# Kernel optimization log

Measured on AMD Instinct MI355X. Metric: run time of the kernel, lower is better.

## Reference

```python
import jax, jax.numpy as jnp
import numpy as np

DIM = 1024
SEQ = 32768
BATCH = 1
MIN_ACTIVE = 0.01
MAX_ACTIVE = 0.1
KMAX = int(MAX_ACTIVE * DIM) + 1  # static upper bound on dynamic k (<= 102)
EPS = 1e-6


def setup_inputs() -> dict:
    key = jax.random.key(0)
    ks = jax.random.split(key, 7)
    h = DIM // 8
    s = 0.02
    return {
        "x": jax.random.normal(ks[0], (BATCH, SEQ, DIM), jnp.float32),
        # complexity_net: Linear(dim, dim//8) -> GELU -> Linear(dim//8, 1) -> Sigmoid
        "w1": jax.random.normal(ks[1], (DIM, h), jnp.float32) * s,
        "b1": jnp.zeros((h,), jnp.float32),
        "w2": jax.random.normal(ks[2], (h, 1), jnp.float32) * s,
        "b2": jnp.zeros((1,), jnp.float32),
        # gate_net: Linear(dim, dim)
        "wg": jax.random.normal(ks[3], (DIM, DIM), jnp.float32) * s,
        "bg": jnp.zeros((DIM,), jnp.float32),
        # running stats (eval mode: used for normalization, not updated)
        "running_mean": jax.random.normal(ks[4], (DIM,), jnp.float32) * 0.1,
        "running_var": jax.random.uniform(ks[5], (DIM,), jnp.float32, minval=0.5, maxval=1.5),
    }


def reference(x, w1, b1, w2, b2, wg, bg, running_mean, running_var):
    # complexity from seq-mean pooled features -> scalar in (0,1)
    pooled = x.mean(axis=1, keepdims=True)                      # (B,1,D)
    hid = jax.nn.gelu(pooled @ w1 + b1, approximate=False)      # torch GELU is exact erf
    complexity = jax.nn.sigmoid(hid @ w2 + b2)                  # (B,1,1)
    active_ratio = MIN_ACTIVE + (MAX_ACTIVE - MIN_ACTIVE) * complexity
    # torch .int() truncates; clamp(min=1). B==1 so k is effectively scalar.
    k = jnp.clip((active_ratio * DIM).astype(jnp.int32), 1, KMAX)  # (B,1,1)

    importance = jnp.abs(x @ wg + bg)                           # (B,S,D)
    importance = (importance - running_mean) / (jnp.sqrt(running_var) + EPS)

    # dynamic-k topk via static-KMAX top_k + threshold at the k-th largest value
    topk_vals, _ = jax.lax.top_k(importance, KMAX)              # (B,S,KMAX)
    idx = jnp.broadcast_to((k - 1).astype(jnp.int32), (x.shape[0], x.shape[1], 1))
    kth = jnp.take_along_axis(topk_vals, idx, axis=-1)          # (B,S,1)
    mask = (importance >= kth).astype(x.dtype)                  # (B,S,D), non-differentiable
    mask = jax.lax.stop_gradient(mask)

    # straight-through combine: forward = x*mask, backward passes grad to all of x
    sparse_x = x * mask + (x - jax.lax.stop_gradient(x)) * (1.0 - mask)

    complexity_mean = complexity.mean()
    active_ratio_mean = active_ratio.mean()
    active_neurons = k.astype(jnp.float32).mean()
    return sparse_x, complexity_mean, active_ratio_mean, active_neurons
```

## Files before the change

### kernel.cpp

```cpp
#include <hip/hip_runtime.h>
#include <cstdint>
#include <cstddef>

#define SEQ 32768
#define DIM 1024
#define HID 128
#define KMAXV 103

using f4 = __attribute__((ext_vector_type(4))) float;
using f2 = __attribute__((ext_vector_type(2))) float;

__global__ __launch_bounds__(256) void pool_partial(const float* __restrict__ x,
                                                    double* __restrict__ part) {
    const int b = blockIdx.x;
    const int t = threadIdx.x;
    const int r0 = b * 128;
    double s0 = 0.0, s1 = 0.0, s2 = 0.0, s3 = 0.0;
    for (int r = 0; r < 128; ++r) {
        const float* row = x + (size_t)(r0 + r) * DIM;
        s0 += (double)row[t];
        s1 += (double)row[t + 256];
        s2 += (double)row[t + 512];
        s3 += (double)row[t + 768];
    }
    double* p = part + (size_t)b * DIM;
    p[t] = s0; p[t + 256] = s1; p[t + 512] = s2; p[t + 768] = s3;
}

__global__ __launch_bounds__(1024) void tiny_net(const double* __restrict__ part,
                                                 const float* __restrict__ w1,
                                                 const float* __restrict__ b1,
                                                 const float* __restrict__ w2,
                                                 const float* __restrict__ b2,
                                                 float* __restrict__ out_scalars,
                                                 int* __restrict__ kout) {
    __shared__ double pooled[DIM];
    __shared__ double hidv[HID];
    const int t = threadIdx.x;

    double s = 0.0;
    for (int b = 0; b < 256; ++b) s += part[(size_t)b * DIM + t];
    pooled[t] = s / (double)SEQ;
    __syncthreads();

    if (t < HID) {
        double h = (double)b1[t];
        for (int d = 0; d < DIM; ++d) h += pooled[d] * (double)w1[d * HID + t];
        h = 0.5 * h * (1.0 + erf(h * 0.70710678118654752440));
        hidv[t] = h;
    }
    __syncthreads();

    if (t == 0) {
        double z = (double)b2[0];
        for (int j = 0; j < HID; ++j) z += hidv[j] * (double)w2[j];
        double c = 1.0 / (1.0 + exp(-z));
        double ar = 0.01 + 0.09 * c;
        int k = (int)(ar * (double)DIM);
        if (k < 1) k = 1;
        if (k > KMAXV) k = KMAXV;
        out_scalars[0] = (float)c;
        out_scalars[1] = (float)ar;
        out_scalars[2] = (float)k;
        *kout = k;
    }
}

#define BM 16
#define CBLOCK 512

__device__ __forceinline__ void fma_step(const float* __restrict__ xp,
                                         f2 w0, f2 w1, f2 w2, f2 w3,
                                         f2 acc[16]) {
#pragma unroll
    for (int m = 0; m < 16; ++m) {
        const f2 xab = *(const f2*)(xp + m * DIM);
        const f2 xcd = *(const f2*)(xp + m * DIM + 2);
        asm("v_pk_fma_f32 %0, %1, %2, %0 op_sel:[0,0,0] op_sel_hi:[0,1,1]"
            : "+v"(acc[m]) : "s"(xab), "v"(w0));
        asm("v_pk_fma_f32 %0, %1, %2, %0 op_sel:[1,0,0] op_sel_hi:[1,1,1]"
            : "+v"(acc[m]) : "s"(xab), "v"(w1));
        asm("v_pk_fma_f32 %0, %1, %2, %0 op_sel:[0,0,0] op_sel_hi:[0,1,1]"
            : "+v"(acc[m]) : "s"(xcd), "v"(w2));
        asm("v_pk_fma_f32 %0, %1, %2, %0 op_sel:[1,0,0] op_sel_hi:[1,1,1]"
            : "+v"(acc[m]) : "s"(xcd), "v"(w3));
    }
}

template<int K0, int K1>
__device__ __forceinline__ void panel_acc(const float* __restrict__ x,
                                          const float* __restrict__ wbase,
                                          int row0, f2 acc[16]) {
#pragma unroll
    for (int m = 0; m < 16; ++m) { acc[m][0] = 0.0f; acc[m][1] = 0.0f; }

    const float* xbase = x + (size_t)row0 * DIM;

    f2 a0 = *(const f2*)(wbase + (size_t)(K0 + 0) * DIM);
    f2 a1 = *(const f2*)(wbase + (size_t)(K0 + 1) * DIM);
    f2 a2 = *(const f2*)(wbase + (size_t)(K0 + 2) * DIM);
    f2 a3 = *(const f2*)(wbase + (size_t)(K0 + 3) * DIM);

    for (int kk0 = K0; kk0 < K1; kk0 += 8) {
        const f2 b0 = *(const f2*)(wbase + (size_t)(kk0 + 4) * DIM);
        const f2 b1 = *(const f2*)(wbase + (size_t)(kk0 + 5) * DIM);
        const f2 b2v = *(const f2*)(wbase + (size_t)(kk0 + 6) * DIM);
        const f2 b3 = *(const f2*)(wbase + (size_t)(kk0 + 7) * DIM);

        fma_step(xbase + kk0, a0, a1, a2, a3, acc);

        const int kn = (kk0 + 8 < K1) ? kk0 + 8 : K0;
        const f2 c0 = *(const f2*)(wbase + (size_t)(kn + 0) * DIM);
        const f2 c1 = *(const f2*)(wbase + (size_t)(kn + 1) * DIM);
        const f2 c2v = *(const f2*)(wbase + (size_t)(kn + 2) * DIM);
        const f2 c3 = *(const f2*)(wbase + (size_t)(kn + 3) * DIM);

        fma_step(xbase + kk0 + 4, b0, b1, b2v, b3, acc);

        a0 = c0; a1 = c1; a2 = c2v; a3 = c3;
    }
}

__global__ __launch_bounds__(CBLOCK) void panel1_kernel(const float* __restrict__ x,
                                                        const float* __restrict__ wg,
                                                        float* __restrict__ out) {
    const int t = threadIdx.x;
    const int c2 = t << 1;
    const int row0 = blockIdx.x * BM;

    f2 pacc[16];
    panel_acc<0, 384>(x, wg + c2, row0, pacc);

#pragma unroll
    for (int m = 0; m < 16; ++m)
        *(f2*)(out + (size_t)(row0 + m) * DIM + c2) = pacc[m];
}

__global__ __launch_bounds__(CBLOCK) void panel2_kernel(const float* __restrict__ x,
                                                        const float* __restrict__ wg,
                                                        float* __restrict__ out) {
    const int t = threadIdx.x;
    const int c2 = t << 1;
    const int row0 = blockIdx.x * BM;

    f2 pacc[16];
    panel_acc<384, 704>(x, wg + c2, row0, pacc);

#pragma unroll
    for (int m = 0; m < 16; ++m) {
        float* op = out + (size_t)(row0 + m) * DIM + c2;
        f2 d = *(const f2*)op;
        d[0] = d[0] + pacc[m][0];
        d[1] = d[1] + pacc[m][1];
        *(f2*)op = d;
    }
}

__global__ __launch_bounds__(CBLOCK) void panel3_kernel(const float* __restrict__ x,
                                                        const float* __restrict__ wg,
                                                        const float* __restrict__ bg,
                                                        const float* __restrict__ rm,
                                                        const float* __restrict__ rv,
                                                        const int* __restrict__ kptr,
                                                        float* __restrict__ out) {
    __shared__ float lbuf[8 * DIM];

    const int t = threadIdx.x;
    const int c2 = t << 1;
    const int row0 = blockIdx.x * BM;

    f2 pacc[16];
    panel_acc<704, 1024>(x, wg + c2, row0, pacc);

    float dot[16][2];
#pragma unroll
    for (int m = 0; m < 16; ++m) {
        const f2 d = *(const f2*)(out + (size_t)(row0 + m) * DIM + c2);
        dot[m][0] = d[0] + pacc[m][0];
        dot[m][1] = d[1] + pacc[m][1];
    }

    const f2 vbg = *(const f2*)(bg + c2);
    const f2 vrm = *(const f2*)(rm + c2);
    const f2 vrv = *(const f2*)(rv + c2);
    f2 vden;
    vden[0] = sqrtf(vrv[0]) + 1e-6f;
    vden[1] = sqrtf(vrv[1]) + 1e-6f;

    f2 imp[16];
#pragma unroll
    for (int m = 0; m < 16; ++m) {
        imp[m][0] = (fabsf(dot[m][0] + vbg[0]) - vrm[0]) / vden[0];
        imp[m][1] = (fabsf(dot[m][1] + vbg[1]) - vrm[1]) / vden[1];
    }

    int kval = *kptr;
    if (kval < 1) kval = 1;
    if (kval > DIM) kval = DIM;

    float (*selbuf)[DIM] = (float (*)[DIM])lbuf;

    for (int ch = 0; ch < 2; ++ch) {
        __syncthreads();
#pragma unroll
        for (int m = 0; m < 8; ++m)
            *(f2*)(&selbuf[m][c2]) = imp[ch * 8 + m];
        __syncthreads();

        const int w = t >> 6;
        const int l = t & 63;
        const size_t srow = (size_t)(row0 + ch * 8 + w);

        unsigned keys[16];
#pragma unroll
        for (int j = 0; j < 4; ++j) {
            const f4 v = *(const f4*)(&selbuf[w][4 * l + 256 * j]);
#pragma unroll
            for (int i = 0; i < 4; ++i) {
                const unsigned u = __float_as_uint(v[i]);
                keys[j * 4 + i] = (u & 0x80000000u) ? ~u : (u | 0x80000000u);
            }
        }

        unsigned pref = 0u;
        for (int b = 31; b >= 0; --b) {
            const unsigned tt = pref | (1u << b);
            int cnt = 0;
#pragma unroll
            for (int j = 0; j < 16; ++j) cnt += (keys[j] >= tt) ? 1 : 0;
#pragma unroll
            for (int off = 32; off >= 1; off >>= 1) cnt += __shfl_xor(cnt, off, 64);
            if (cnt >= kval) pref = tt;
        }

        const float* xr = x + srow * DIM;
        float* orow = out + srow * DIM;
#pragma unroll
        for (int j = 0; j < 4; ++j) {
            const f4 xv = *(const f4*)(xr + 4 * l + 256 * j);
            f4 o;
#pragma unroll
            for (int i = 0; i < 4; ++i) o[i] = (keys[j * 4 + i] >= pref) ? xv[i] : 0.0f;
            *(f4*)(orow + 4 * l + 256 * j) = o;
        }
    }
}

extern "C" void kernel_launch(void* const* d_in, const int* in_sizes, int n_in,
                              void* d_out, int out_size, void* d_ws, size_t ws_size,
                              hipStream_t stream) {
    const float* x  = (const float*)d_in[0];
    const float* w1 = (const float*)d_in[1];
    const float* b1 = (const float*)d_in[2];
    const float* w2 = (const float*)d_in[3];
    const float* b2 = (const float*)d_in[4];
    const float* wg = (const float*)d_in[5];
    const float* bg = (const float*)d_in[6];
    const float* rm = (const float*)d_in[7];
    const float* rv = (const float*)d_in[8];
    float* out = (float*)d_out;

    double* part = (double*)d_ws;
    int* kptr = (int*)((char*)d_ws + (size_t)256 * DIM * sizeof(double));

    pool_partial<<<256, 256, 0, stream>>>(x, part);
    tiny_net<<<1, 1024, 0, stream>>>(part, w1, b1, w2, b2,
                                     out + (size_t)SEQ * DIM, kptr);
    panel1_kernel<<<SEQ / BM, CBLOCK, 0, stream>>>(x, wg, out);
    panel2_kernel<<<SEQ / BM, CBLOCK, 0, stream>>>(x, wg, out);
    panel3_kernel<<<SEQ / BM, CBLOCK, 0, stream>>>(x, wg, bg, rm, rv, kptr, out);
}
```

Before: 0.9999 ms.

## Fuse three K-panel GEMM kernels into one kernel with 1024-thread blocks

Replaces three panel kernels with one fused kernel. The kernels previously wrote and reread partial dot products through the output buffer between launches; the fused kernel keeps the accumulation in registers and runs the normalization and top-k selection in the same kernel. Block size doubles to 1024 threads, with two 8-row groups per block, so each thread holds 8 accumulators instead of 16 and loads x as float4. Costs include lower occupancy per CU and the x loads possibly becoming scalar loads from a uniform row group, so the register and scheduling behavior may change.

```diff
diff --git a/kernel.cpp b/kernel.cpp
--- a/kernel.cpp
+++ b/kernel.cpp
@@ -67,15 +67,16 @@
 }
 
 #define BM 16
-#define CBLOCK 512
-
-__device__ __forceinline__ void fma_step(const float* __restrict__ xp,
-                                         f2 w0, f2 w1, f2 w2, f2 w3,
-                                         f2 acc[16]) {
-#pragma unroll
-    for (int m = 0; m < 16; ++m) {
-        const f2 xab = *(const f2*)(xp + m * DIM);
-        const f2 xcd = *(const f2*)(xp + m * DIM + 2);
+#define CBLOCK 1024
+
+__device__ __forceinline__ void fma_step2(const float* __restrict__ xp,
+                                          f2 w0, f2 w1, f2 w2, f2 w3,
+                                          f2 acc[8]) {
+#pragma unroll
+    for (int m = 0; m < 8; ++m) {
+        const f4 xq = *(const f4*)(xp + m * DIM);
+        const f2 xab = __builtin_shufflevector(xq, xq, 0, 1);
+        const f2 xcd = __builtin_shufflevector(xq, xq, 2, 3);
         asm("v_pk_fma_f32 %0, %1, %2, %0 op_sel:[0,0,0] op_sel_hi:[0,1,1]"
             : "+v"(acc[m]) : "s"(xab), "v"(w0));
         asm("v_pk_fma_f32 %0, %1, %2, %0 op_sel:[1,0,0] op_sel_hi:[1,1,1]"
@@ -88,13 +89,11 @@
 }
 
 template<int K0, int K1>
-__device__ __forceinline__ void panel_acc(const float* __restrict__ x,
-                                          const float* __restrict__ wbase,
-                                          int row0, f2 acc[16]) {
-#pragma unroll
-    for (int m = 0; m < 16; ++m) { acc[m][0] = 0.0f; acc[m][1] = 0.0f; }
-
-    const float* xbase = x + (size_t)row0 * DIM;
+__device__ __forceinline__ void panel_acc2(const float* __restrict__ xbase,
+                                           const float* __restrict__ wbase,
+                                           f2 acc[8]) {
+#pragma unroll
+    for (int m = 0; m < 8; ++m) { acc[m][0] = 0.0f; acc[m][1] = 0.0f; }
 
     f2 a0 = *(const f2*)(wbase + (size_t)(K0 + 0) * DIM);
     f2 a1 = *(const f2*)(wbase + (size_t)(K0 + 1) * DIM);
@@ -107,7 +106,7 @@
         const f2 b2v = *(const f2*)(wbase + (size_t)(kk0 + 6) * DIM);
         const f2 b3 = *(const f2*)(wbase + (size_t)(kk0 + 7) * DIM);
 
-        fma_step(xbase + kk0, a0, a1, a2, a3, acc);
+        fma_step2(xbase + kk0, a0, a1, a2, a3, acc);
 
         const int kn = (kk0 + 8 < K1) ? kk0 + 8 : K0;
         const f2 c0 = *(const f2*)(wbase + (size_t)(kn + 0) * DIM);
@@ -115,69 +114,48 @@
         const f2 c2v = *(const f2*)(wbase + (size_t)(kn + 2) * DIM);
         const f2 c3 = *(const f2*)(wbase + (size_t)(kn + 3) * DIM);
 
-        fma_step(xbase + kk0 + 4, b0, b1, b2v, b3, acc);
+        fma_step2(xbase + kk0 + 4, b0, b1, b2v, b3, acc);
 
         a0 = c0; a1 = c1; a2 = c2v; a3 = c3;
     }
 }
 
-__global__ __launch_bounds__(CBLOCK) void panel1_kernel(const float* __restrict__ x,
-                                                        const float* __restrict__ wg,
-                                                        float* __restrict__ out) {
+__global__ __launch_bounds__(CBLOCK) void fused_kernel(const float* __restrict__ x,
+                                                       const float* __restrict__ wg,
+                                                       const float* __restrict__ bg,
+                                                       const float* __restrict__ rm,
+                                                       const float* __restrict__ rv,
+                                                       const int* __restrict__ kptr,
+                                                       float* __restrict__ out) {
+    __shared__ float selbuf[BM][DIM];
+
     const int t = threadIdx.x;
-    const int c2 = t << 1;
-    const int row0 = blockIdx.x * BM;
-
-    f2 pacc[16];
-    panel_acc<0, 384>(x, wg + c2, row0, pacc);
-
-#pragma unroll
-    for (int m = 0; m < 16; ++m)
-        *(f2*)(out + (size_t)(row0 + m) * DIM + c2) = pacc[m];
-}
-
-__global__ __launch_bounds__(CBLOCK) void panel2_kernel(const float* __restrict__ x,
-                                                        const float* __restrict__ wg,
-                                                        float* __restrict__ out) {
-    const int t = threadIdx.x;
-    const int c2 = t << 1;
-    const int row0 = blockIdx.x * BM;
-
-    f2 pacc[16];
-    panel_acc<384, 704>(x, wg + c2, row0, pacc);
-
-#pragma unroll
-    for (int m = 0; m < 16; ++m) {
-        float* op = out + (size_t)(row0 + m) * DIM + c2;
-        f2 d = *(const f2*)op;
-        d[0] = d[0] + pacc[m][0];
-        d[1] = d[1] + pacc[m][1];
-        *(f2*)op = d;
-    }
-}
-
-__global__ __launch_bounds__(CBLOCK) void panel3_kernel(const float* __restrict__ x,
-                                                        const float* __restrict__ wg,
-                                                        const float* __restrict__ bg,
-                                                        const float* __restrict__ rm,
-                                                        const float* __restrict__ rv,
-                                                        const int* __restrict__ kptr,
-                                                        float* __restrict__ out) {
-    __shared__ float lbuf[8 * DIM];
-
-    const int t = threadIdx.x;
-    const int c2 = t << 1;
-    const int row0 = blockIdx.x * BM;
-
-    f2 pacc[16];
-    panel_acc<704, 1024>(x, wg + c2, row0, pacc);
-
-    float dot[16][2];
-#pragma unroll
-    for (int m = 0; m < 16; ++m) {
-        const f2 d = *(const f2*)(out + (size_t)(row0 + m) * DIM + c2);
-        dot[m][0] = d[0] + pacc[m][0];
-        dot[m][1] = d[1] + pacc[m][1];
+    const int c2 = (t & 511) << 1;
+    const int rg = __builtin_amdgcn_readfirstlane(t >> 9);
+    const int row0 = blockIdx.x * BM + rg * 8;
+
+    const float* xbase = x + (size_t)row0 * DIM;
+    const float* wbase = wg + c2;
+
+    f2 pacc[8];
+    f2 dot[8];
+
+    panel_acc2<0, 384>(xbase, wbase, pacc);
+#pragma unroll
+    for (int m = 0; m < 8; ++m) dot[m] = pacc[m];
+
+    panel_acc2<384, 704>(xbase, wbase, pacc);
+#pragma unroll
+    for (int m = 0; m < 8; ++m) {
+        dot[m][0] = dot[m][0] + pacc[m][0];
+        dot[m][1] = dot[m][1] + pacc[m][1];
+    }
+
+    panel_acc2<704, 1024>(xbase, wbase, pacc);
+#pragma unroll
+    for (int m = 0; m < 8; ++m) {
+        dot[m][0] = dot[m][0] + pacc[m][0];
+        dot[m][1] = dot[m][1] + pacc[m][1];
     }
 
     const f2 vbg = *(const f2*)(bg + c2);
@@ -187,62 +165,55 @@
     vden[0] = sqrtf(vrv[0]) + 1e-6f;
     vden[1] = sqrtf(vrv[1]) + 1e-6f;
 
-    f2 imp[16];
-#pragma unroll
-    for (int m = 0; m < 16; ++m) {
-        imp[m][0] = (fabsf(dot[m][0] + vbg[0]) - vrm[0]) / vden[0];
-        imp[m][1] = (fabsf(dot[m][1] + vbg[1]) - vrm[1]) / vden[1];
+#pragma unroll
+    for (int m = 0; m < 8; ++m) {
+        f2 v;
+        v[0] = (fabsf(dot[m][0] + vbg[0]) - vrm[0]) / vden[0];
+        v[1] = (fabsf(dot[m][1] + vbg[1]) - vrm[1]) / vden[1];
+        *(f2*)(&selbuf[rg * 8 + m][c2]) = v;
     }
 
     int kval = *kptr;
     if (kval < 1) kval = 1;
     if (kval > DIM) kval = DIM;
 
-    float (*selbuf)[DIM] = (float (*)[DIM])lbuf;
-
-    for (int ch = 0; ch < 2; ++ch) {
-        __syncthreads();
-#pragma unroll
-        for (int m = 0; m < 8; ++m)
-            *(f2*)(&selbuf[m][c2]) = imp[ch * 8 + m];
-        __syncthreads();
-
-        const int w = t >> 6;
-        const int l = t & 63;
-        const size_t srow = (size_t)(row0 + ch * 8 + w);
-
-        unsigned keys[16];
-#pragma unroll
-        for (int j = 0; j < 4; ++j) {
-            const f4 v = *(const f4*)(&selbuf[w][4 * l + 256 * j]);
-#pragma unroll
-            for (int i = 0; i < 4; ++i) {
-                const unsigned u = __float_as_uint(v[i]);
-                keys[j * 4 + i] = (u & 0x80000000u) ? ~u : (u | 0x80000000u);
-            }
+    __syncthreads();
+
+    const int w = t >> 6;
+    const int l = t & 63;
+    const size_t srow = (size_t)(blockIdx.x * BM + w);
+
+    unsigned keys[16];
+#pragma unroll
+    for (int j = 0; j < 4; ++j) {
+        const f4 v = *(const f4*)(&selbuf[w][4 * l + 256 * j]);
+#pragma unroll
+        for (int i = 0; i < 4; ++i) {
+            const unsigned u = __float_as_uint(v[i]);
+            keys[j * 4 + i] = (u & 0x80000000u) ? ~u : (u | 0x80000000u);
         }
-
-        unsigned pref = 0u;
-        for (int b = 31; b >= 0; --b) {
-            const unsigned tt = pref | (1u << b);
-            int cnt = 0;
-#pragma unroll
-            for (int j = 0; j < 16; ++j) cnt += (keys[j] >= tt) ? 1 : 0;
-#pragma unroll
-            for (int off = 32; off >= 1; off >>= 1) cnt += __shfl_xor(cnt, off, 64);
-            if (cnt >= kval) pref = tt;
-        }
-
-        const float* xr = x + srow * DIM;
-        float* orow = out + srow * DIM;
-#pragma unroll
-        for (int j = 0; j < 4; ++j) {
-            const f4 xv = *(const f4*)(xr + 4 * l + 256 * j);
-            f4 o;
-#pragma unroll
-            for (int i = 0; i < 4; ++i) o[i] = (keys[j * 4 + i] >= pref) ? xv[i] : 0.0f;
-            *(f4*)(orow + 4 * l + 256 * j) = o;
-        }
+    }
+
+    unsigned pref = 0u;
+    for (int b = 31; b >= 0; --b) {
+        const unsigned tt = pref | (1u << b);
+        int cnt = 0;
+#pragma unroll
+        for (int j = 0; j < 16; ++j) cnt += (keys[j] >= tt) ? 1 : 0;
+#pragma unroll
+        for (int off = 32; off >= 1; off >>= 1) cnt += __shfl_xor(cnt, off, 64);
+        if (cnt >= kval) pref = tt;
+    }
+
+    const float* xr = x + srow * DIM;
+    float* orow = out + srow * DIM;
+#pragma unroll
+    for (int j = 0; j < 4; ++j) {
+        const f4 xv = *(const f4*)(xr + 4 * l + 256 * j);
+        f4 o;
+#pragma unroll
+        for (int i = 0; i < 4; ++i) o[i] = (keys[j * 4 + i] >= pref) ? xv[i] : 0.0f;
+        *(f4*)(orow + 4 * l + 256 * j) = o;
     }
 }
 
@@ -266,7 +237,5 @@
     pool_partial<<<256, 256, 0, stream>>>(x, part);
     tiny_net<<<1, 1024, 0, stream>>>(part, w1, b1, w2, b2,
                                      out + (size_t)SEQ * DIM, kptr);
-    panel1_kernel<<<SEQ / BM, CBLOCK, 0, stream>>>(x, wg, out);
-    panel2_kernel<<<SEQ / BM, CBLOCK, 0, stream>>>(x, wg, out);
-    panel3_kernel<<<SEQ / BM, CBLOCK, 0, stream>>>(x, wg, bg, rm, rv, kptr, out);
-}
+    fused_kernel<<<SEQ / BM, CBLOCK, 0, stream>>>(x, wg, bg, rm, rv, kptr, out);
+}
```

Result: slower. 1.213 ms (+21.3%).
